# Kernel optimization log

Hardware: AMD Instinct MI355X
Metric: run time of the kernel (lower is better)

Reference implementation:

```python
import jax, jax.numpy as jnp
import numpy as np

B, IN, OUT = 8192, 4096, 2048  # OUT must equal 32*64 per betta/gamma sizes


def setup_inputs() -> dict:
    key = jax.random.key(0)
    kx, kw = jax.random.split(key, 2)
    X = jax.random.normal(kx, (B, IN), dtype=jnp.float32)
    # xavier-uniform-like init for W
    limit = float(np.sqrt(6.0 / (IN + OUT)))
    W = jax.random.uniform(kw, (IN, OUT), minval=-limit, maxval=limit, dtype=jnp.float32)
    absmean = jnp.abs(W).mean(axis=0)
    alpha = jnp.abs(W).mean()          # scalar, >= 0
    betta = absmean[:32]               # (32,), >= 0
    gamma = absmean[32:96]             # (64,), >= 0
    return {"X": X, "W": W, "alpha": alpha, "betta": betta, "gamma": gamma}


def reference(X, W, alpha, betta, gamma):
    # module applies relu_ to alpha/betta/gamma data before the functional call
    alpha = jax.nn.relu(alpha)
    betta = jax.nn.relu(betta)
    gamma = jax.nn.relu(gamma)
    X_bin = jnp.sign(X)                # (B, IN)
    W_bin = jnp.sign(W)                # (IN, OUT)
    # scale[i*64+j] = alpha * betta[i] * gamma[j] -> (OUT,)
    scale = (alpha * jnp.outer(betta, gamma)).reshape(-1)
    return (X_bin @ W_bin) * scale     # (B, OUT)
```

## Files before the change

### kernel.cpp

```cpp
#include <hip/hip_runtime.h>


#define M_DIM 8192
#define K_DIM 4096
#define N_DIM 2048
#define KB    (K_DIM / 2)
#define NT    (K_DIM / 256)

typedef int i32x4 __attribute__((ext_vector_type(4)));
typedef int i32x8 __attribute__((ext_vector_type(8)));
typedef float f32x16 __attribute__((ext_vector_type(16)));

__device__ __forceinline__ unsigned int nib4(float x) {
  unsigned int s = (__float_as_uint(x) >> 28) & 0x8u;
  return x == 0.0f ? 0u : (0x2u | s);
}

__device__ __forceinline__ void gload_lds16(const void* g, void* lds) {
  __builtin_amdgcn_global_load_lds(
      (const __attribute__((address_space(1))) unsigned int*)g,
      (__attribute__((address_space(3))) unsigned int*)lds, 16, 0, 0);
}

__device__ __forceinline__ i32x8 pad8(i32x4 v) {
  i32x8 r;
  r[0] = v[0]; r[1] = v[1]; r[2] = v[2]; r[3] = v[3];
  r[4] = 0; r[5] = 0; r[6] = 0; r[7] = 0;
  return r;
}

__global__ void binX4_kernel(const float* __restrict__ X,
                             unsigned int* __restrict__ Xq, int n16) {
  int stride = gridDim.x * blockDim.x;
  for (int i = blockIdx.x * blockDim.x + threadIdx.x; i < n16; i += stride) {
    size_t base = (size_t)i * 16;
    unsigned int lo = 0, hi = 0;
#pragma unroll
    for (int j = 0; j < 2; ++j) {
      float4 v0 = *(const float4*)&X[base + j * 8];
      float4 v1 = *(const float4*)&X[base + j * 8 + 4];
      unsigned int p = 0;
      p |= nib4(v0.x) << 0;  p |= nib4(v0.y) << 4;
      p |= nib4(v0.z) << 8;  p |= nib4(v0.w) << 12;
      p |= nib4(v1.x) << 16; p |= nib4(v1.y) << 20;
      p |= nib4(v1.z) << 24; p |= nib4(v1.w) << 28;
      if (j == 0) lo = p; else hi = p;
    }
    uint2 r; r.x = lo; r.y = hi;
    *(uint2*)&Xq[(size_t)i * 2] = r;
  }
}

__global__ void binW4_kernel(const float* __restrict__ W,
                             unsigned short* __restrict__ Wq) {
  __shared__ float tile[32][33];
  const int n0 = blockIdx.x * 32;
  const int k0 = blockIdx.y * 32;
  const int t = threadIdx.x;
  const int tc = t & 31;
  const int tr = t >> 5;
#pragma unroll
  for (int i = 0; i < 32; i += 8)
    tile[tr + i][tc] = W[(size_t)(k0 + tr + i) * N_DIM + n0 + tc];
  __syncthreads();
  const int r = t >> 3;
  const int c = t & 7;
  unsigned int b0 = nib4(tile[c * 4 + 0][r]) | (nib4(tile[c * 4 + 1][r]) << 4);
  unsigned int b1 = nib4(tile[c * 4 + 2][r]) | (nib4(tile[c * 4 + 3][r]) << 4);
  Wq[(size_t)(n0 + r) * (KB / 2) + (k0 >> 2) + c] = (unsigned short)(b0 | (b1 << 8));
}

__device__ __forceinline__ void stage_tile(const unsigned char* __restrict__ src,
                                           unsigned char* lds, int t) {
#pragma unroll
  for (int p = 0; p < 4; ++p) {
    int c = p * 512 + t;
    int r = c >> 3;
    int gg = (c & 7) ^ (r & 7);
    gload_lds16(src + (size_t)r * KB + gg * 16, lds + c * 16);
  }
}

__global__ __launch_bounds__(512, 2) void gemm_fp4_kernel(
    const unsigned char* __restrict__ Aq,
    const unsigned char* __restrict__ Bq,
    const float* __restrict__ alpha,
    const float* __restrict__ betta,
    const float* __restrict__ gamma,
    float* __restrict__ C) {
  __shared__ __align__(16) unsigned char smem[131072];

  const int t = threadIdx.x;
  const int lane = t & 63;
  const int l31 = lane & 31;
  const int lhi = lane >> 5;
  const int w = t >> 6;
  const int wr = w >> 2;
  const int wc = w & 3;

  const int bid = blockIdx.x;
  const int swz = (bid & 7) * 32 + (bid >> 3);
  const int bn = swz >> 5;
  const int bm = swz & 31;
  const int row0 = bm * 256;
  const int col0 = bn * 256;

  const unsigned char* Asrc = Aq + (size_t)row0 * KB;
  const unsigned char* Bsrc = Bq + (size_t)col0 * KB;

  f32x16 acc[4][2];
#pragma unroll
  for (int fm = 0; fm < 4; ++fm)
#pragma unroll
    for (int fn = 0; fn < 2; ++fn)
#pragma unroll
      for (int r = 0; r < 16; ++r) acc[fm][fn][r] = 0.f;

  stage_tile(Asrc, &smem[0], t);
  stage_tile(Bsrc, &smem[32768], t);
  asm volatile("s_waitcnt vmcnt(0)" ::: "memory");
  __builtin_amdgcn_s_barrier();

  for (int kt = 0; kt < NT; ++kt) {
    const int cur = kt & 1;
    const unsigned char* pA = &smem[cur * 65536];
    const unsigned char* pB = pA + 32768;
    const int nktb = (kt + 1) * 128;

#pragma unroll
    for (int kk = 0; kk < 4; ++kk) {
      const int g = kk * 2 + lhi;
      i32x4 a4[4], b4[2];
#pragma unroll
      for (int fm = 0; fm < 4; ++fm) {
        const int rr = wr * 128 + fm * 32 + l31;
        a4[fm] = *(const i32x4*)&pA[rr * 128 + ((g ^ (rr & 7)) * 16)];
      }
#pragma unroll
      for (int fn = 0; fn < 2; ++fn) {
        const int rr = wc * 64 + fn * 32 + l31;
        b4[fn] = *(const i32x4*)&pB[rr * 128 + ((g ^ (rr & 7)) * 16)];
      }
      if (kk == 0 && kt + 1 < NT)
        stage_tile(Asrc + nktb, &smem[(cur ^ 1) * 65536], t);
      if (kk == 1 && kt + 1 < NT)
        stage_tile(Bsrc + nktb, &smem[(cur ^ 1) * 65536 + 32768], t);

      __builtin_amdgcn_s_barrier();
      asm volatile("s_waitcnt lgkmcnt(0)" ::: "memory");
      __builtin_amdgcn_sched_barrier(0);
      __builtin_amdgcn_s_setprio(1);
#pragma unroll
      for (int fm = 0; fm < 4; ++fm) {
        i32x8 av = pad8(a4[fm]);
#pragma unroll
        for (int fn = 0; fn < 2; ++fn)
          acc[fm][fn] = __builtin_amdgcn_mfma_scale_f32_32x32x64_f8f6f4(
              av, pad8(b4[fn]), acc[fm][fn], 4, 4,
              0, 0x7F7F7F7F, 0, 0x7F7F7F7F);
      }
      __builtin_amdgcn_s_setprio(0);
      if (kk < 3) __builtin_amdgcn_s_barrier();
    }
    asm volatile("s_waitcnt vmcnt(0)" ::: "memory");
    __builtin_amdgcn_s_barrier();
  }

  const float ra = fmaxf(alpha[0], 0.0f);
#pragma unroll
  for (int fn = 0; fn < 2; ++fn) {
    const int col = col0 + wc * 64 + fn * 32 + l31;
    const float sc = ra * fmaxf(betta[col >> 6], 0.0f) * fmaxf(gamma[col & 63], 0.0f);
#pragma unroll
    for (int fm = 0; fm < 4; ++fm) {
      const int rbase = row0 + wr * 128 + fm * 32 + 4 * lhi;
#pragma unroll
      for (int r = 0; r < 16; ++r) {
        const int row = rbase + (r & 3) + 8 * (r >> 2);
        C[(size_t)row * N_DIM + col] = acc[fm][fn][r] * sc;
      }
    }
  }
}

extern "C" void kernel_launch(void* const* d_in, const int* in_sizes, int n_in,
                              void* d_out, int out_size, void* d_ws, size_t ws_size,
                              hipStream_t stream) {
  const float* X = (const float*)d_in[0];
  const float* W = (const float*)d_in[1];
  const float* alpha = (const float*)d_in[2];
  const float* betta = (const float*)d_in[3];
  const float* gamma = (const float*)d_in[4];
  float* out = (float*)d_out;

  unsigned char* Xq = (unsigned char*)d_ws;
  unsigned char* Wq = Xq + (size_t)M_DIM * KB;

  binX4_kernel<<<2048, 256, 0, stream>>>(X, (unsigned int*)Xq,
                                         (M_DIM * K_DIM) / 16);
  binW4_kernel<<<dim3(N_DIM / 32, K_DIM / 32), 256, 0, stream>>>(
      W, (unsigned short*)Wq);
  gemm_fp4_kernel<<<(M_DIM / 256) * (N_DIM / 256), 512, 0, stream>>>(
      Xq, Wq, alpha, betta, gamma, out);
}
```

Baseline: 75.51 us.

## Fuse binarization kernels and pre-tile FP4 operands into MFMA-ready panel layout

```diff
diff --git a/kernel.cpp b/kernel.cpp
--- a/kernel.cpp
+++ b/kernel.cpp
@@ -4,8 +4,9 @@
 #define M_DIM 8192
 #define K_DIM 4096
 #define N_DIM 2048
-#define KB    (K_DIM / 2)
 #define NT    (K_DIM / 256)
+#define TILE_BYTES 32768
+#define PANEL_BYTES (NT * TILE_BYTES)
 
 typedef int i32x4 __attribute__((ext_vector_type(4)));
 typedef int i32x8 __attribute__((ext_vector_type(8)));
@@ -14,6 +15,13 @@
 __device__ __forceinline__ unsigned int nib4(float x) {
   unsigned int s = (__float_as_uint(x) >> 28) & 0x8u;
   return x == 0.0f ? 0u : (0x2u | s);
+}
+
+__device__ __forceinline__ unsigned int pack8(const float* f) {
+  unsigned int p = 0;
+#pragma unroll
+  for (int j = 0; j < 8; ++j) p |= nib4(f[j]) << (4 * j);
+  return p;
 }
 
 __device__ __forceinline__ void gload_lds16(const void* g, void* lds) {
@@ -29,45 +37,53 @@
   return r;
 }
 
-__global__ void binX4_kernel(const float* __restrict__ X,
-                             unsigned int* __restrict__ Xq, int n16) {
-  int stride = gridDim.x * blockDim.x;
-  for (int i = blockIdx.x * blockDim.x + threadIdx.x; i < n16; i += stride) {
-    size_t base = (size_t)i * 16;
-    unsigned int lo = 0, hi = 0;
-#pragma unroll
-    for (int j = 0; j < 2; ++j) {
-      float4 v0 = *(const float4*)&X[base + j * 8];
-      float4 v1 = *(const float4*)&X[base + j * 8 + 4];
-      unsigned int p = 0;
-      p |= nib4(v0.x) << 0;  p |= nib4(v0.y) << 4;
-      p |= nib4(v0.z) << 8;  p |= nib4(v0.w) << 12;
-      p |= nib4(v1.x) << 16; p |= nib4(v1.y) << 20;
-      p |= nib4(v1.z) << 24; p |= nib4(v1.w) << 28;
-      if (j == 0) lo = p; else hi = p;
-    }
-    uint2 r; r.x = lo; r.y = hi;
-    *(uint2*)&Xq[(size_t)i * 2] = r;
-  }
-}
-
-__global__ void binW4_kernel(const float* __restrict__ W,
-                             unsigned short* __restrict__ Wq) {
-  __shared__ float tile[32][33];
-  const int n0 = blockIdx.x * 32;
-  const int k0 = blockIdx.y * 32;
+__global__ __launch_bounds__(256) void binXW_kernel(
+    const float* __restrict__ X, const float* __restrict__ W,
+    unsigned char* __restrict__ Xq, unsigned char* __restrict__ Wq) {
+  __shared__ float tile[32][257];
   const int t = threadIdx.x;
-  const int tc = t & 31;
-  const int tr = t >> 5;
-#pragma unroll
-  for (int i = 0; i < 32; i += 8)
-    tile[tr + i][tc] = W[(size_t)(k0 + tr + i) * N_DIM + n0 + tc];
-  __syncthreads();
-  const int r = t >> 3;
-  const int c = t & 7;
-  unsigned int b0 = nib4(tile[c * 4 + 0][r]) | (nib4(tile[c * 4 + 1][r]) << 4);
-  unsigned int b1 = nib4(tile[c * 4 + 2][r]) | (nib4(tile[c * 4 + 3][r]) << 4);
-  Wq[(size_t)(n0 + r) * (KB / 2) + (k0 >> 2) + c] = (unsigned short)(b0 | (b1 << 8));
+  const int bid = blockIdx.x;
+
+  if (bid < 512) {
+    const int p = bid >> 4;
+    const int kt = bid & 15;
+    const float* Xrow = X + (size_t)(p * 256 + t) * K_DIM + kt * 256;
+    unsigned char* dst = Xq + (size_t)p * PANEL_BYTES + kt * TILE_BYTES;
+#pragma unroll
+    for (int s = 0; s < 8; ++s) {
+      float f[32];
+#pragma unroll
+      for (int i = 0; i < 8; ++i)
+        *(float4*)&f[i * 4] = *(const float4*)&Xrow[s * 32 + i * 4];
+      uint4 gq;
+      gq.x = pack8(f + 0);  gq.y = pack8(f + 8);
+      gq.z = pack8(f + 16); gq.w = pack8(f + 24);
+      *(uint4*)&dst[(s * 256 + t) * 16] = gq;
+    }
+  } else {
+    const int idx = bid - 512;
+    const int q = idx >> 4;
+    const int kt = idx & 15;
+    unsigned char* dst = Wq + (size_t)q * PANEL_BYTES + kt * TILE_BYTES;
+    for (int s = 0; s < 8; ++s) {
+#pragma unroll
+      for (int it = 0; it < 8; ++it) {
+        int row = it * 4 + (t >> 6);
+        int col4 = (t & 63) * 4;
+        *(float4*)&tile[row][col4] =
+            *(const float4*)&W[(size_t)(kt * 256 + s * 32 + row) * N_DIM + q * 256 + col4];
+      }
+      __syncthreads();
+      float f[32];
+#pragma unroll
+      for (int k = 0; k < 32; ++k) f[k] = tile[k][t];
+      uint4 gq;
+      gq.x = pack8(f + 0);  gq.y = pack8(f + 8);
+      gq.z = pack8(f + 16); gq.w = pack8(f + 24);
+      *(uint4*)&dst[(s * 256 + t) * 16] = gq;
+      __syncthreads();
+    }
+  }
 }
 
 __device__ __forceinline__ void stage_tile(const unsigned char* __restrict__ src,
@@ -75,9 +91,7 @@
 #pragma unroll
   for (int p = 0; p < 4; ++p) {
     int c = p * 512 + t;
-    int r = c >> 3;
-    int gg = (c & 7) ^ (r & 7);
-    gload_lds16(src + (size_t)r * KB + gg * 16, lds + c * 16);
+    gload_lds16(src + c * 16, lds + c * 16);
   }
 }
 
@@ -99,14 +113,13 @@
   const int wc = w & 3;
 
   const int bid = blockIdx.x;
-  const int swz = (bid & 7) * 32 + (bid >> 3);
-  const int bn = swz >> 5;
-  const int bm = swz & 31;
+  const int bn = bid & 7;
+  const int bm = bid >> 3;
   const int row0 = bm * 256;
   const int col0 = bn * 256;
 
-  const unsigned char* Asrc = Aq + (size_t)row0 * KB;
-  const unsigned char* Bsrc = Bq + (size_t)col0 * KB;
+  const unsigned char* Abase = Aq + (size_t)bm * PANEL_BYTES;
+  const unsigned char* Bbase = Bq + (size_t)bn * PANEL_BYTES;
 
   f32x16 acc[4][2];
 #pragma unroll
@@ -116,8 +129,8 @@
 #pragma unroll
       for (int r = 0; r < 16; ++r) acc[fm][fn][r] = 0.f;
 
-  stage_tile(Asrc, &smem[0], t);
-  stage_tile(Bsrc, &smem[32768], t);
+  stage_tile(Abase, &smem[0], t);
+  stage_tile(Bbase, &smem[32768], t);
   asm volatile("s_waitcnt vmcnt(0)" ::: "memory");
   __builtin_amdgcn_s_barrier();
 
@@ -125,26 +138,22 @@
     const int cur = kt & 1;
     const unsigned char* pA = &smem[cur * 65536];
     const unsigned char* pB = pA + 32768;
-    const int nktb = (kt + 1) * 128;
 
 #pragma unroll
     for (int kk = 0; kk < 4; ++kk) {
       const int g = kk * 2 + lhi;
       i32x4 a4[4], b4[2];
 #pragma unroll
-      for (int fm = 0; fm < 4; ++fm) {
-        const int rr = wr * 128 + fm * 32 + l31;
-        a4[fm] = *(const i32x4*)&pA[rr * 128 + ((g ^ (rr & 7)) * 16)];
-      }
-#pragma unroll
-      for (int fn = 0; fn < 2; ++fn) {
-        const int rr = wc * 64 + fn * 32 + l31;
-        b4[fn] = *(const i32x4*)&pB[rr * 128 + ((g ^ (rr & 7)) * 16)];
-      }
+      for (int fm = 0; fm < 4; ++fm)
+        a4[fm] = *(const i32x4*)&pA[(g * 256 + wr * 128 + fm * 32 + l31) * 16];
+#pragma unroll
+      for (int fn = 0; fn < 2; ++fn)
+        b4[fn] = *(const i32x4*)&pB[(g * 256 + wc * 64 + fn * 32 + l31) * 16];
+
       if (kk == 0 && kt + 1 < NT)
-        stage_tile(Asrc + nktb, &smem[(cur ^ 1) * 65536], t);
+        stage_tile(Abase + (kt + 1) * TILE_BYTES, &smem[(cur ^ 1) * 65536], t);
       if (kk == 1 && kt + 1 < NT)
-        stage_tile(Bsrc + nktb, &smem[(cur ^ 1) * 65536 + 32768], t);
+        stage_tile(Bbase + (kt + 1) * TILE_BYTES, &smem[(cur ^ 1) * 65536 + 32768], t);
 
       __builtin_amdgcn_s_barrier();
       asm volatile("s_waitcnt lgkmcnt(0)" ::: "memory");
@@ -160,7 +169,6 @@
               0, 0x7F7F7F7F, 0, 0x7F7F7F7F);
       }
       __builtin_amdgcn_s_setprio(0);
-      if (kk < 3) __builtin_amdgcn_s_barrier();
     }
     asm volatile("s_waitcnt vmcnt(0)" ::: "memory");
     __builtin_amdgcn_s_barrier();
@@ -194,12 +202,9 @@
   float* out = (float*)d_out;
 
   unsigned char* Xq = (unsigned char*)d_ws;
-  unsigned char* Wq = Xq + (size_t)M_DIM * KB;
-
-  binX4_kernel<<<2048, 256, 0, stream>>>(X, (unsigned int*)Xq,
-                                         (M_DIM * K_DIM) / 16);
-  binW4_kernel<<<dim3(N_DIM / 32, K_DIM / 32), 256, 0, stream>>>(
-      W, (unsigned short*)Wq);
+  unsigned char* Wq = Xq + (size_t)(M_DIM / 256) * PANEL_BYTES;
+
+  binXW_kernel<<<640, 256, 0, stream>>>(X, W, Xq, Wq);
   gemm_fp4_kernel<<<(M_DIM / 256) * (N_DIM / 256), 512, 0, stream>>>(
       Xq, Wq, alpha, betta, gamma, out);
 }
```

Result: slower. 81.28 us (+7.6%).
